# Optimization experiments

Hardware: AMD Instinct MI355X
Metric: run time of the kernel (lower is better)

## Reference

```python
import jax, jax.numpy as jnp
import numpy as np

N, E, DIN, H, C, ED = 50000, 500000, 264, 4, 32, 16
HID = H * C   # 128
OUT = 128
NEG_SLOPE = 0.2
LN_EPS = 1e-5


def _ln(x, g, b):
    mu = jnp.mean(x, axis=-1, keepdims=True)
    var = jnp.mean((x - mu) ** 2, axis=-1, keepdims=True)
    return (x - mu) * jax.lax.rsqrt(var + LN_EPS) * g + b


def _segment_softmax(scores, seg, num_segments):
    # scores: (E, H), seg: (E,) destination node ids
    m = jax.ops.segment_max(scores, seg, num_segments=num_segments)
    m = jnp.where(jnp.isfinite(m), m, 0.0)
    ex = jnp.exp(scores - m[seg])
    s = jax.ops.segment_sum(ex, seg, num_segments=num_segments)
    return ex / (s[seg] + 1e-16)


def _gatv2(x, src, dst, edge_attr, Wl, bl, Wr, br, We, att, bias):
    # GATv2Conv (PyG semantics): lin_l -> source, lin_r -> target, lin_edge (no bias)
    n = x.shape[0]
    xl = (x @ Wl + bl).reshape(n, H, C)          # source transform
    xr = (x @ Wr + br).reshape(n, H, C)          # target transform
    ee = (edge_attr @ We).reshape(-1, H, C)      # (E, H, C)
    m = xl[src] + xr[dst] + ee                   # per-edge pre-activation
    g = jnp.where(m > 0, m, NEG_SLOPE * m)       # leaky_relu(0.2)
    score = jnp.einsum('ehc,hc->eh', g, att)     # (E, H)
    alpha = _segment_softmax(score, dst, n)      # softmax over in-edges of each dst
    msg = xl[src] * alpha[..., None]             # (E, H, C)
    out = jax.ops.segment_sum(msg, dst, num_segments=n)
    return out.reshape(n, HID) + bias


def setup_inputs() -> dict:
    key = jax.random.key(0)
    ks = jax.random.split(key, 16)
    r = lambda k, s: jax.random.normal(k, s, dtype=jnp.float32) * 0.05
    return {
        'x': jax.random.normal(ks[0], (N, DIN), jnp.float32),
        'edge_attr': jax.random.normal(ks[1], (E, ED), jnp.float32),
        'Wl1': r(ks[2], (DIN, HID)), 'bl1': jnp.zeros((HID,), jnp.float32),
        'Wr1': r(ks[3], (DIN, HID)), 'br1': jnp.zeros((HID,), jnp.float32),
        'We1': r(ks[4], (ED, HID)), 'att1': r(ks[5], (H, C)), 'bias1': jnp.zeros((HID,), jnp.float32),
        'Wl2': r(ks[6], (HID, HID)), 'bl2': jnp.zeros((HID,), jnp.float32),
        'Wr2': r(ks[7], (HID, HID)), 'br2': jnp.zeros((HID,), jnp.float32),
        'We2': r(ks[8], (ED, HID)), 'att2': r(ks[9], (H, C)), 'bias2': jnp.zeros((HID,), jnp.float32),
        'Wres': r(ks[10], (DIN, HID)), 'bres': jnp.zeros((HID,), jnp.float32),
        'Wout': r(ks[11], (HID, OUT)), 'bout': jnp.zeros((OUT,), jnp.float32),
        'g1': jnp.ones((HID,), jnp.float32), 'bn1': jnp.zeros((HID,), jnp.float32),
        'g2': jnp.ones((HID,), jnp.float32), 'bn2': jnp.zeros((HID,), jnp.float32),
        'go': jnp.ones((OUT,), jnp.float32), 'bo': jnp.zeros((OUT,), jnp.float32),
        'edge_index': jax.random.randint(ks[12], (2, E), 0, N, dtype=jnp.int32),
    }


def reference(x, edge_attr, Wl1, bl1, Wr1, br1, We1, att1, bias1,
              Wl2, bl2, Wr2, br2, We2, att2, bias2,
              Wres, bres, Wout, bout, g1, bn1, g2, bn2, go, bo, edge_index):
    src, dst = edge_index[0], edge_index[1]
    residual = x @ Wres + bres
    h = _gatv2(x, src, dst, edge_attr, Wl1, bl1, Wr1, br1, We1, att1, bias1)
    h = jax.nn.elu(h)
    h = _ln(h + residual, g1, bn1)
    residual = h
    h = _gatv2(h, src, dst, edge_attr, Wl2, bl2, Wr2, br2, We2, att2, bias2)
    h = jax.nn.elu(h)
    h = _ln(h + residual, g2, bn2)
    context = _ln(h @ Wout + bout, go, bo)
    return context
```

## Files before the change

kernel.cpp:

```cpp
#include <hip/hip_runtime.h>
#include <hip/hip_bf16.h>
#include <math.h>
#include <stdint.h>

#define NN 50000
#define NE 500000
#define DIN 264
#define KP1 288
#define HID 128
#define EDIM 16
#define GS_LD 136

typedef __attribute__((ext_vector_type(8))) short short8;
typedef __attribute__((ext_vector_type(4))) float f32x4;

__device__ __forceinline__ short f2bf(float v) {
    union { float f; unsigned u; } x; x.f = v;
    unsigned r = x.u + 0x7fff + ((x.u >> 16) & 1);
    return (short)(r >> 16);
}
__device__ __forceinline__ float bf2f(short v) {
    union { float f; unsigned u; } x;
    x.u = ((unsigned)(unsigned short)v) << 16;
    return x.f;
}
__device__ __forceinline__ float bflo(unsigned u) {
    union { float f; unsigned u; } x; x.u = u << 16; return x.f;
}
__device__ __forceinline__ float bfhi(unsigned u) {
    union { float f; unsigned u; } x; x.u = u & 0xffff0000u; return x.f;
}
__device__ __forceinline__ unsigned pk2bf(float a, float b) {
    return (unsigned)(unsigned short)f2bf(a) | ((unsigned)(unsigned short)f2bf(b) << 16);
}

__device__ __forceinline__ void gload_lds16(const void* g, void* l) {
    __builtin_amdgcn_global_load_lds(
        (const __attribute__((address_space(1))) unsigned int*)g,
        (__attribute__((address_space(3))) unsigned int*)l, 16, 0, 0);
}

__global__ void k_count(const int* __restrict__ dst, int* __restrict__ cnt) {
    int e = blockIdx.x * blockDim.x + threadIdx.x;
    if (e < NE) atomicAdd(&cnt[dst[e]], 1);
}

__global__ __launch_bounds__(256) void k_scan1(const int* __restrict__ cnt,
                                               int* __restrict__ off, int* __restrict__ bsum) {
    __shared__ int buf[256];
    int b = blockIdx.x, t = threadIdx.x;
    int i = b * 256 + t;
    int v = (i < NN) ? cnt[i] : 0;
    buf[t] = v; __syncthreads();
    for (int s = 1; s < 256; s <<= 1) {
        int u = (t >= s) ? buf[t - s] : 0; __syncthreads();
        buf[t] += u; __syncthreads();
    }
    if (i < NN) off[i + 1] = buf[t];
    if (t == 255) bsum[b] = buf[255];
}

__global__ void k_scan2(int* __restrict__ bsum, int nb) {
    __shared__ int buf[256];
    int t = threadIdx.x;
    int o = (t < nb) ? bsum[t] : 0;
    buf[t] = o; __syncthreads();
    for (int s = 1; s < 256; s <<= 1) {
        int u = (t >= s) ? buf[t - s] : 0; __syncthreads();
        buf[t] += u; __syncthreads();
    }
    if (t < nb) bsum[t] = buf[t] - o;
}

__global__ void k_scan3c(int* __restrict__ off, const int* __restrict__ bsum,
                         int* __restrict__ cur) {
    int j = blockIdx.x * 256 + threadIdx.x;
    if (j > NN) return;
    int v = (j == 0) ? 0 : off[j] + bsum[(j - 1) >> 8];
    off[j] = v;
    if (j < NN) cur[j] = v;
}

__global__ void k_scatter(const int* __restrict__ src, const int* __restrict__ dst,
                          int* __restrict__ cur, int* __restrict__ srcp,
                          int* __restrict__ dstp, int* __restrict__ ey) {
    int e = blockIdx.x * blockDim.x + threadIdx.x;
    if (e < NE) {
        int d = dst[e];
        int p = atomicAdd(&cur[d], 1);
        srcp[p] = src[e];
        dstp[p] = d;
        ey[p] = e;
    }
}

__global__ void k_cvt_x(const float* __restrict__ x, short* __restrict__ xb) {
    int idx = blockIdx.x * 256 + threadIdx.x;
    if (idx >= NN * KP1) return;
    int i = idx / KP1, k = idx - i * KP1;
    xb[idx] = (k < DIN) ? f2bf(x[(size_t)i * DIN + k]) : (short)0;
}

__global__ void k_prep_w(const float* __restrict__ Wl1, const float* __restrict__ Wr1,
                         const float* __restrict__ Wres, const float* __restrict__ Wl2,
                         const float* __restrict__ Wr2, const float* __restrict__ Wout,
                         const float* __restrict__ bl1, const float* __restrict__ br1,
                         const float* __restrict__ bres, const float* __restrict__ bl2,
                         const float* __restrict__ br2,
                         const float* __restrict__ We1, const float* __restrict__ We2,
                         const float* __restrict__ att1, const float* __restrict__ att2,
                         short* __restrict__ Wt1, short* __restrict__ Wt2,
                         short* __restrict__ Wt3, float* __restrict__ bcat1,
                         float* __restrict__ bcat2,
                         short* __restrict__ WeT1, short* __restrict__ WeT2,
                         short* __restrict__ attB1, short* __restrict__ attB2) {
    int idx = blockIdx.x * 256 + threadIdx.x;
    if (idx < 384 * KP1) {
        int n = idx / KP1, k = idx - n * KP1;
        float v = 0.f;
        if (k < DIN) {
            const float* W = (n < 128) ? Wl1 : ((n < 256) ? Wr1 : Wres);
            v = W[(size_t)k * 128 + (n & 127)];
        }
        Wt1[idx] = f2bf(v);
        return;
    }
    idx -= 384 * KP1;
    if (idx < 256 * 128) {
        int n = idx >> 7, k = idx & 127;
        const float* W = (n < 128) ? Wl2 : Wr2;
        Wt2[idx] = f2bf(W[(size_t)k * 128 + (n & 127)]);
        return;
    }
    idx -= 256 * 128;
    if (idx < 128 * 128) {
        int n = idx >> 7, k = idx & 127;
        Wt3[idx] = f2bf(Wout[(size_t)k * 128 + n]);
        return;
    }
    idx -= 128 * 128;
    if (idx < 384) {
        bcat1[idx] = (idx < 128) ? bl1[idx] : ((idx < 256) ? br1[idx - 128] : bres[idx - 256]);
        return;
    }
    idx -= 384;
    if (idx < 256) {
        bcat2[idx] = (idx < 128) ? bl2[idx] : br2[idx - 128];
        return;
    }
    idx -= 256;
    if (idx < 128 * 32) {
        int n = idx >> 5, k = idx & 31;
        WeT1[idx] = (k < EDIM) ? f2bf(We1[(size_t)k * 128 + n]) : (short)0;
        return;
    }
    idx -= 128 * 32;
    if (idx < 128 * 32) {
        int n = idx >> 5, k = idx & 31;
        WeT2[idx] = (k < EDIM) ? f2bf(We2[(size_t)k * 128 + n]) : (short)0;
        return;
    }
    idx -= 128 * 32;
    if (idx < 16 * 128) {
        int n = idx >> 7, k = idx & 127;
        attB1[idx] = (n == (k >> 5)) ? f2bf(att1[k]) : (short)0;
        return;
    }
    idx -= 16 * 128;
    if (idx < 16 * 128) {
        int n = idx >> 7, k = idx & 127;
        attB2[idx] = (n == (k >> 5)) ? f2bf(att2[k]) : (short)0;
    }
}

__global__ __launch_bounds__(256) void k_gather_ea(const int* __restrict__ ey,
                                                   const float* __restrict__ ea,
                                                   short* __restrict__ eaperm) {
    int pos = blockIdx.x * 256 + threadIdx.x;
    if (pos >= NE) return;
    int e = ey[pos];
    const float4* r = (const float4*)(ea + (size_t)e * EDIM);
    float4 v0 = r[0], v1 = r[1], v2 = r[2], v3 = r[3];
    uint4 w0 = make_uint4(pk2bf(v0.x, v0.y), pk2bf(v0.z, v0.w),
                          pk2bf(v1.x, v1.y), pk2bf(v1.z, v1.w));
    uint4 w1 = make_uint4(pk2bf(v2.x, v2.y), pk2bf(v2.z, v2.w),
                          pk2bf(v3.x, v3.y), pk2bf(v3.z, v3.w));
    uint4* o = (uint4*)(eaperm + (size_t)pos * 32);
    o[0] = w0; o[1] = w1;
    o[2] = make_uint4(0, 0, 0, 0);
    o[3] = make_uint4(0, 0, 0, 0);
}

template <bool BF16OUT>
__global__ __launch_bounds__(256) void k_mfma_gemm(const short* __restrict__ A,
                                                   const short* __restrict__ Bt,
                                                   const float* __restrict__ bias,
                                                   float* __restrict__ Cf,
                                                   short* __restrict__ Cb,
                                                   int M, int Kpad, int NS) {
    __shared__ short As[128 * 32];
    __shared__ short Bs[128 * 32];
    int t = threadIdx.x;
    int lane = t & 63, wid = t >> 6;
    int wm = (wid & 1) * 64, wn = (wid >> 1) * 64;
    int cl = lane & 15, quad = lane >> 4;
    int row0 = blockIdx.x * 128;
    int col0 = blockIdx.y * 128;

    f32x4 acc[4][4];
#pragma unroll
    for (int i = 0; i < 4; ++i)
#pragma unroll
        for (int j = 0; j < 4; ++j) acc[i][j] = (f32x4)0.f;

    for (int k0 = 0; k0 < Kpad; k0 += 32) {
#pragma unroll
        for (int r = 0; r < 2; ++r) {
            int c = t + r * 256;
            int m = c >> 2;
            int row = row0 + m; if (row >= M) row = M - 1;
            const char* ga = (const char*)A + ((size_t)row * Kpad + k0) * 2 + (c & 3) * 16;
            gload_lds16(ga, (char*)As + c * 16);
            int n = col0 + m;
            const char* gb = (const char*)Bt + ((size_t)n * Kpad + k0) * 2 + (c & 3) * 16;
            gload_lds16(gb, (char*)Bs + c * 16);
        }
        __syncthreads();

        short8 a[4], b[4];
#pragma unroll
        for (int mi = 0; mi < 4; ++mi)
            a[mi] = *(const short8*)&As[(wm + mi * 16 + cl) * 32 + quad * 8];
#pragma unroll
        for (int ni = 0; ni < 4; ++ni)
            b[ni] = *(const short8*)&Bs[(wn + ni * 16 + cl) * 32 + quad * 8];
#pragma unroll
        for (int mi = 0; mi < 4; ++mi)
#pragma unroll
            for (int ni = 0; ni < 4; ++ni)
                acc[mi][ni] = __builtin_amdgcn_mfma_f32_16x16x32_bf16(a[mi], b[ni], acc[mi][ni], 0, 0, 0);
        __syncthreads();
    }

#pragma unroll
    for (int mi = 0; mi < 4; ++mi)
#pragma unroll
        for (int ni = 0; ni < 4; ++ni) {
            int col = col0 + wn + ni * 16 + cl;
            float bv = bias[col];
#pragma unroll
            for (int r = 0; r < 4; ++r) {
                int row = row0 + wm + mi * 16 + quad * 4 + r;
                if (row < M) {
                    float v = acc[mi][ni][r] + bv;
                    if (BF16OUT) Cb[(size_t)row * NS + col] = f2bf(v);
                    else         Cf[(size_t)row * NS + col] = v;
                }
            }
        }
}

__global__ __launch_bounds__(256) void k_gemm_ln(const short* __restrict__ A,
                                                 const short* __restrict__ Bt,
                                                 const float* __restrict__ bias,
                                                 const float* __restrict__ gamma,
                                                 const float* __restrict__ beta,
                                                 float* __restrict__ out, int M) {
    __shared__ short As[128 * 32];
    __shared__ short Bs[128 * 32];
    __shared__ float redS[128][2];
    int t = threadIdx.x;
    int lane = t & 63, wid = t >> 6;
    int wm = (wid & 1) * 64, wn = (wid >> 1) * 64;
    int cl = lane & 15, quad = lane >> 4;
    int row0 = blockIdx.x * 128;
    int wh = wid >> 1;

    f32x4 acc[4][4];
#pragma unroll
    for (int i = 0; i < 4; ++i)
#pragma unroll
        for (int j = 0; j < 4; ++j) acc[i][j] = (f32x4)0.f;

    for (int k0 = 0; k0 < 128; k0 += 32) {
#pragma unroll
        for (int r = 0; r < 2; ++r) {
            int c = t + r * 256;
            int m = c >> 2;
            int row = row0 + m; if (row >= M) row = M - 1;
            const char* ga = (const char*)A + ((size_t)row * 128 + k0) * 2 + (c & 3) * 16;
            gload_lds16(ga, (char*)As + c * 16);
            const char* gb = (const char*)Bt + ((size_t)m * 128 + k0) * 2 + (c & 3) * 16;
            gload_lds16(gb, (char*)Bs + c * 16);
        }
        __syncthreads();

        short8 a[4], b[4];
#pragma unroll
        for (int mi = 0; mi < 4; ++mi)
            a[mi] = *(const short8*)&As[(wm + mi * 16 + cl) * 32 + quad * 8];
#pragma unroll
        for (int ni = 0; ni < 4; ++ni)
            b[ni] = *(const short8*)&Bs[(wn + ni * 16 + cl) * 32 + quad * 8];
#pragma unroll
        for (int mi = 0; mi < 4; ++mi)
#pragma unroll
            for (int ni = 0; ni < 4; ++ni)
                acc[mi][ni] = __builtin_amdgcn_mfma_f32_16x16x32_bf16(a[mi], b[ni], acc[mi][ni], 0, 0, 0);
        __syncthreads();
    }

    float bv[4], gv[4], bev[4];
#pragma unroll
    for (int ni = 0; ni < 4; ++ni) {
        int col = wn + ni * 16 + cl;
        bv[ni] = bias[col]; gv[ni] = gamma[col]; bev[ni] = beta[col];
    }

    float s[4][4];
#pragma unroll
    for (int mi = 0; mi < 4; ++mi)
#pragma unroll
        for (int r = 0; r < 4; ++r) {
            float v = (acc[mi][0][r] + bv[0]) + (acc[mi][1][r] + bv[1]) +
                      (acc[mi][2][r] + bv[2]) + (acc[mi][3][r] + bv[3]);
            v += __shfl_xor(v, 1, 64);
            v += __shfl_xor(v, 2, 64);
            v += __shfl_xor(v, 4, 64);
            v += __shfl_xor(v, 8, 64);
            s[mi][r] = v;
        }
    if (cl == 0) {
#pragma unroll
        for (int mi = 0; mi < 4; ++mi)
#pragma unroll
            for (int r = 0; r < 4; ++r)
                redS[wm + mi * 16 + quad * 4 + r][wh] = s[mi][r];
    }
    __syncthreads();
    float mean[4][4];
#pragma unroll
    for (int mi = 0; mi < 4; ++mi)
#pragma unroll
        for (int r = 0; r < 4; ++r) {
            int rl = wm + mi * 16 + quad * 4 + r;
            mean[mi][r] = (redS[rl][0] + redS[rl][1]) * (1.f / 128.f);
        }
    __syncthreads();

#pragma unroll
    for (int mi = 0; mi < 4; ++mi)
#pragma unroll
        for (int r = 0; r < 4; ++r) {
            float q = 0.f;
#pragma unroll
            for (int ni = 0; ni < 4; ++ni) {
                float d = acc[mi][ni][r] + bv[ni] - mean[mi][r];
                q = fmaf(d, d, q);
            }
            q += __shfl_xor(q, 1, 64);
            q += __shfl_xor(q, 2, 64);
            q += __shfl_xor(q, 4, 64);
            q += __shfl_xor(q, 8, 64);
            s[mi][r] = q;
        }
    if (cl == 0) {
#pragma unroll
        for (int mi = 0; mi < 4; ++mi)
#pragma unroll
            for (int r = 0; r < 4; ++r)
                redS[wm + mi * 16 + quad * 4 + r][wh] = s[mi][r];
    }
    __syncthreads();

#pragma unroll
    for (int mi = 0; mi < 4; ++mi)
#pragma unroll
        for (int r = 0; r < 4; ++r) {
            int rl = wm + mi * 16 + quad * 4 + r;
            int row = row0 + rl;
            if (row < M) {
                float rstd = rsqrtf((redS[rl][0] + redS[rl][1]) * (1.f / 128.f) + 1e-5f);
#pragma unroll
                for (int ni = 0; ni < 4; ++ni) {
                    int col = wn + ni * 16 + cl;
                    float d = acc[mi][ni][r] + bv[ni] - mean[mi][r];
                    out[(size_t)row * 128 + col] = fmaf(d * rstd, gv[ni], bev[ni]);
                }
            }
        }
}

template <int STRIDE>
__global__ __launch_bounds__(256) void k_edge_score(const short* __restrict__ eaperm,
                                                    const short* __restrict__ WeT,
                                                    const short* __restrict__ attB,
                                                    const int* __restrict__ srcp,
                                                    const int* __restrict__ dstp,
                                                    const short* __restrict__ C,
                                                    float* __restrict__ pe) {
    __shared__ short As[128 * 32];
    __shared__ short Bs[128 * 32];
    __shared__ short Gs[128 * GS_LD];
    __shared__ short Ab[16 * 128];
    __shared__ int sS[128], sD[128];
    int t = threadIdx.x;
    int lane = t & 63, wid = t >> 6;
    int wm = (wid & 1) * 64, wn = (wid >> 1) * 64;
    int cl = lane & 15, quad = lane >> 4;
    long e0 = (long)blockIdx.x * 128;

    if (t < 128) {
        long ep = e0 + t; if (ep >= NE) ep = NE - 1;
        sS[t] = srcp[ep];
        sD[t] = dstp[ep];
    }
    ((uint4*)Ab)[t] = ((const uint4*)attB)[t];

#pragma unroll
    for (int r = 0; r < 2; ++r) {
        int c = t + r * 256;
        int m = c >> 2;
        long row = e0 + m; if (row >= NE) row = NE - 1;
        const char* ga = (const char*)eaperm + row * 64 + (c & 3) * 16;
        gload_lds16(ga, (char*)As + c * 16);
        const char* gb = (const char*)WeT + (size_t)m * 64 + (c & 3) * 16;
        gload_lds16(gb, (char*)Bs + c * 16);
    }
    __syncthreads();

    f32x4 acc[4][4];
#pragma unroll
    for (int i = 0; i < 4; ++i)
#pragma unroll
        for (int j = 0; j < 4; ++j) acc[i][j] = (f32x4)0.f;
    {
        short8 a[4], b[4];
#pragma unroll
        for (int mi = 0; mi < 4; ++mi)
            a[mi] = *(const short8*)&As[(wm + mi * 16 + cl) * 32 + quad * 8];
#pragma unroll
        for (int ni = 0; ni < 4; ++ni)
            b[ni] = *(const short8*)&Bs[(wn + ni * 16 + cl) * 32 + quad * 8];
#pragma unroll
        for (int mi = 0; mi < 4; ++mi)
#pragma unroll
            for (int ni = 0; ni < 4; ++ni)
                acc[mi][ni] = __builtin_amdgcn_mfma_f32_16x16x32_bf16(a[mi], b[ni], acc[mi][ni], 0, 0, 0);
    }

#pragma unroll
    for (int mi = 0; mi < 4; ++mi) {
#pragma unroll
        for (int r = 0; r < 4; ++r) {
            int eloc = wm + mi * 16 + quad * 4 + r;
            const short* xlr = C + (size_t)sS[eloc] * STRIDE;
            const short* xrr = C + (size_t)sD[eloc] * STRIDE + 128;
#pragma unroll
            for (int ni = 0; ni < 4; ++ni) {
                int f = wn + ni * 16 + cl;
                float g = acc[mi][ni][r] + bf2f(xlr[f]) + bf2f(xrr[f]);
                g = fmaxf(g, 0.2f * g);
                Gs[eloc * GS_LD + f] = f2bf(g);
            }
        }
    }
    __syncthreads();

    f32x4 sacc[2];
    sacc[0] = (f32x4)0.f; sacc[1] = (f32x4)0.f;
    int em0 = wid * 32;
#pragma unroll
    for (int mt = 0; mt < 2; ++mt) {
#pragma unroll
        for (int ks = 0; ks < 4; ++ks) {
            short8 ag = *(const short8*)&Gs[(em0 + mt * 16 + cl) * GS_LD + ks * 32 + quad * 8];
            short8 bg = *(const short8*)&Ab[cl * 128 + ks * 32 + quad * 8];
            sacc[mt] = __builtin_amdgcn_mfma_f32_16x16x32_bf16(ag, bg, sacc[mt], 0, 0, 0);
        }
    }

    if (cl < 4) {
#pragma unroll
        for (int mt = 0; mt < 2; ++mt) {
#pragma unroll
            for (int r = 0; r < 4; ++r) {
                long epos = e0 + em0 + mt * 16 + quad * 4 + r;
                if (epos < NE) pe[epos * 4 + cl] = __expf(sacc[mt][r]);
            }
        }
    }
}

template <int STRIDE>
__global__ __launch_bounds__(256) void k_fused_agg(const int* __restrict__ off,
                                                   const int* __restrict__ srcp,
                                                   const float* __restrict__ pe,
                                                   const short* __restrict__ C,
                                                   const short* __restrict__ resid, int rstride,
                                                   const float* __restrict__ bias,
                                                   const float* __restrict__ gamma,
                                                   const float* __restrict__ beta,
                                                   short* __restrict__ outb) {
    int t = threadIdx.x;
    int w = t >> 6, l = t & 63;
    int f0 = (l >> 4) * 32 + (l & 15) * 2;
    int fp = f0 >> 1;
    int hd = l >> 4;

    float2 bs2 = ((const float2*)bias)[fp];
    float2 gv = ((const float2*)gamma)[fp];
    float2 bev = ((const float2*)beta)[fp];

    int n0 = (blockIdx.x * 4 + w) * 4;
    int nend = n0 + 4; if (nend > NN) nend = NN;

    for (int i = n0; i < nend; ++i) {
        unsigned rp = *(const unsigned*)&resid[(size_t)i * rstride + f0];
        int b0 = off[i], b1 = off[i + 1];

        float lA = 0.f, aA0 = 0.f, aA1 = 0.f;
        float lB = 0.f, aB0 = 0.f, aB1 = 0.f;
        int pos = b0;
        int sA = 0, sB = 0; float pA = 0.f, pB = 0.f;
        bool have = (pos + 2 <= b1);
        if (have) {
            sA = srcp[pos]; sB = srcp[pos + 1];
            pA = pe[(size_t)pos * 4 + hd]; pB = pe[(size_t)(pos + 1) * 4 + hd];
        }
        while (have) {
            bool haven = (pos + 4 <= b1);
            int nsA = 0, nsB = 0; float npA = 0.f, npB = 0.f;
            if (haven) {
                nsA = srcp[pos + 2]; nsB = srcp[pos + 3];
                npA = pe[(size_t)(pos + 2) * 4 + hd]; npB = pe[(size_t)(pos + 3) * 4 + hd];
            }
            unsigned xlA = *(const unsigned*)&C[(size_t)sA * STRIDE + f0];
            unsigned xlB = *(const unsigned*)&C[(size_t)sB * STRIDE + f0];
            lA += pA; lB += pB;
            aA0 = fmaf(pA, bflo(xlA), aA0);
            aA1 = fmaf(pA, bfhi(xlA), aA1);
            aB0 = fmaf(pB, bflo(xlB), aB0);
            aB1 = fmaf(pB, bfhi(xlB), aB1);
            pos += 2;
            sA = nsA; sB = nsB; pA = npA; pB = npB;
            have = haven;
        }
        if (pos < b1) {
            int s1 = srcp[pos];
            float p1 = pe[(size_t)pos * 4 + hd];
            unsigned xlv = *(const unsigned*)&C[(size_t)s1 * STRIDE + f0];
            lA += p1;
            aA0 = fmaf(p1, bflo(xlv), aA0);
            aA1 = fmaf(p1, bfhi(xlv), aA1);
        }
        float l_run = lA + lB;
        float acc0 = aA0 + aB0, acc1 = aA1 + aB1;

        float inv = 1.f / (l_run + 1e-16f);
        float o0 = fmaf(acc0, inv, bs2.x);
        float o1 = fmaf(acc1, inv, bs2.y);
        o0 = o0 > 0.f ? o0 : (__expf(o0) - 1.f);
        o1 = o1 > 0.f ? o1 : (__expf(o1) - 1.f);
        float v0 = o0 + bflo(rp), v1 = o1 + bfhi(rp);
        float s = v0 + v1;
#pragma unroll
        for (int o = 32; o > 0; o >>= 1) s += __shfl_xor(s, o, 64);
        float mean = s * (1.f / 128.f);
        float d0 = v0 - mean, d1 = v1 - mean;
        float q = fmaf(d0, d0, d1 * d1);
#pragma unroll
        for (int o = 32; o > 0; o >>= 1) q += __shfl_xor(q, o, 64);
        float rstd = rsqrtf(q * (1.f / 128.f) + 1e-5f);
        float r0 = fmaf(d0 * rstd, gv.x, bev.x);
        float r1 = fmaf(d1 * rstd, gv.y, bev.y);
        unsigned op = (unsigned)(unsigned short)f2bf(r0) |
                      (((unsigned)(unsigned short)f2bf(r1)) << 16);
        *(unsigned*)&outb[(size_t)i * 128 + f0] = op;
    }
}

extern "C" void kernel_launch(void* const* d_in, const int* in_sizes, int n_in,
                              void* d_out, int out_size, void* d_ws, size_t ws_size,
                              hipStream_t stream) {
    (void)in_sizes; (void)n_in; (void)out_size; (void)ws_size;
    const float* x     = (const float*)d_in[0];
    const float* ea    = (const float*)d_in[1];
    const float* Wl1   = (const float*)d_in[2];
    const float* bl1   = (const float*)d_in[3];
    const float* Wr1   = (const float*)d_in[4];
    const float* br1   = (const float*)d_in[5];
    const float* We1   = (const float*)d_in[6];
    const float* att1  = (const float*)d_in[7];
    const float* bias1 = (const float*)d_in[8];
    const float* Wl2   = (const float*)d_in[9];
    const float* bl2   = (const float*)d_in[10];
    const float* Wr2   = (const float*)d_in[11];
    const float* br2   = (const float*)d_in[12];
    const float* We2   = (const float*)d_in[13];
    const float* att2  = (const float*)d_in[14];
    const float* bias2 = (const float*)d_in[15];
    const float* Wres  = (const float*)d_in[16];
    const float* bres  = (const float*)d_in[17];
    const float* Wout  = (const float*)d_in[18];
    const float* bout  = (const float*)d_in[19];
    const float* g1    = (const float*)d_in[20];
    const float* bn1   = (const float*)d_in[21];
    const float* g2    = (const float*)d_in[22];
    const float* bn2   = (const float*)d_in[23];
    const float* go    = (const float*)d_in[24];
    const float* bo    = (const float*)d_in[25];
    const int*   ei    = (const int*)d_in[26];
    const int* srcv = ei;
    const int* dstv = ei + NE;
    float* outp = (float*)d_out;

    char* p = (char*)d_ws;
    auto carve = [&](size_t bytes) {
        char* r = p;
        p += (bytes + 255) & ~(size_t)255;
        return r;
    };
    short* xb    = (short*)carve((size_t)NN * KP1 * 2);
    short* Wt1   = (short*)carve((size_t)384 * KP1 * 2);
    short* Wt2   = (short*)carve((size_t)256 * 128 * 2);
    short* Wt3   = (short*)carve((size_t)128 * 128 * 2);
    short* WeT1  = (short*)carve((size_t)128 * 32 * 2);
    short* WeT2  = (short*)carve((size_t)128 * 32 * 2);
    short* attB1 = (short*)carve((size_t)16 * 128 * 2);
    short* attB2 = (short*)carve((size_t)16 * 128 * 2);
    float* bcat1 = (float*)carve(384 * 4);
    float* bcat2 = (float*)carve(256 * 4);
    short* C1    = (short*)carve((size_t)NN * 384 * 2);
    short* h1b   = (short*)carve((size_t)NN * 128 * 2);
    short* h2b   = (short*)carve((size_t)NN * 128 * 2);
    int* off     = (int*)carve((size_t)(NN + 1) * 4);
    int* cur     = (int*)carve((size_t)NN * 4);
    int* bsum    = (int*)carve(256 * 4);
    int* srcp    = (int*)carve((size_t)NE * 4);
    int* dstp    = (int*)carve((size_t)NE * 4);
    int* ey      = (int*)carve((size_t)NE * 4);
    short* eaperm = (short*)carve((size_t)NE * 32 * 2);
    float* pe    = (float*)carve((size_t)NE * 4 * 4);

    short* C2 = C1;

    const int NB = (NN + 255) / 256;

    hipMemsetAsync(cur, 0, (size_t)NN * 4, stream);
    k_count<<<(NE + 255) / 256, 256, 0, stream>>>(dstv, cur);
    k_scan1<<<NB, 256, 0, stream>>>(cur, off, bsum);
    k_scan2<<<1, 256, 0, stream>>>(bsum, NB);
    k_scan3c<<<(NN + 256) / 256, 256, 0, stream>>>(off, bsum, cur);
    k_scatter<<<(NE + 255) / 256, 256, 0, stream>>>(srcv, dstv, cur, srcp, dstp, ey);

    k_cvt_x<<<((size_t)NN * KP1 + 255) / 256, 256, 0, stream>>>(x, xb);
    int prep_total = 384 * KP1 + 256 * 128 + 128 * 128 + 384 + 256 + 2 * 128 * 32 + 2 * 16 * 128;
    k_prep_w<<<(prep_total + 255) / 256, 256, 0, stream>>>(Wl1, Wr1, Wres, Wl2, Wr2, Wout,
                                                           bl1, br1, bres, bl2, br2,
                                                           We1, We2, att1, att2,
                                                           Wt1, Wt2, Wt3, bcat1, bcat2,
                                                           WeT1, WeT2, attB1, attB2);
    k_gather_ea<<<(NE + 255) / 256, 256, 0, stream>>>(ey, ea, eaperm);

    int mb  = (NN + 127) / 128;
    int ebk = (NE + 127) / 128;
    int gagg = (NN + 15) / 16;

    k_mfma_gemm<true><<<dim3(mb, 3), 256, 0, stream>>>(xb, Wt1, bcat1, nullptr, C1, NN, KP1, 384);
    k_edge_score<384><<<ebk, 256, 0, stream>>>(eaperm, WeT1, attB1, srcp, dstp, C1, pe);
    k_fused_agg<384><<<gagg, 256, 0, stream>>>(off, srcp, pe, C1,
                                               C1 + 256, 384, bias1, g1, bn1, h1b);
    k_mfma_gemm<true><<<dim3(mb, 2), 256, 0, stream>>>(h1b, Wt2, bcat2, nullptr, C2, NN, 128, 256);
    k_edge_score<256><<<ebk, 256, 0, stream>>>(eaperm, WeT2, attB2, srcp, dstp, C2, pe);
    k_fused_agg<256><<<gagg, 256, 0, stream>>>(off, srcp, pe, C2,
                                               h1b, 128, bias2, g2, bn2, h2b);
    k_gemm_ln<<<mb, 256, 0, stream>>>(h2b, Wt3, bout, go, bo, outp, NN);
}
```

Before: 508.7 us.

## Compute edge scores in registers via transposed MFMA, drop LDS staging

The edge-score kernel now computes the transposed product (features × edges) so each lane holds contiguous features of one edge. It loads operands directly from global memory instead of staging them in LDS. The attention dot product is done with FMAs and cross-quad shuffles rather than a second MFMA over an LDS buffer of bf16 activations, which removes both __syncthreads and the intermediate bf16 rounding. Gathered xl/xr rows are read as 4-wide vectors. The risk is more uncoalesced global loads per lane and more shuffle work.

```diff
diff --git a/kernel.cpp b/kernel.cpp
--- a/kernel.cpp
+++ b/kernel.cpp
@@ -9,7 +9,6 @@
 #define KP1 288
 #define HID 128
 #define EDIM 16
-#define GS_LD 136
 
 typedef __attribute__((ext_vector_type(8))) short short8;
 typedef __attribute__((ext_vector_type(4))) float f32x4;
@@ -108,12 +107,10 @@
                          const float* __restrict__ bres, const float* __restrict__ bl2,
                          const float* __restrict__ br2,
                          const float* __restrict__ We1, const float* __restrict__ We2,
-                         const float* __restrict__ att1, const float* __restrict__ att2,
                          short* __restrict__ Wt1, short* __restrict__ Wt2,
                          short* __restrict__ Wt3, float* __restrict__ bcat1,
                          float* __restrict__ bcat2,
-                         short* __restrict__ WeT1, short* __restrict__ WeT2,
-                         short* __restrict__ attB1, short* __restrict__ attB2) {
+                         short* __restrict__ WeT1, short* __restrict__ WeT2) {
     int idx = blockIdx.x * 256 + threadIdx.x;
     if (idx < 384 * KP1) {
         int n = idx / KP1, k = idx - n * KP1;
@@ -158,18 +155,6 @@
     if (idx < 128 * 32) {
         int n = idx >> 5, k = idx & 31;
         WeT2[idx] = (k < EDIM) ? f2bf(We2[(size_t)k * 128 + n]) : (short)0;
-        return;
-    }
-    idx -= 128 * 32;
-    if (idx < 16 * 128) {
-        int n = idx >> 7, k = idx & 127;
-        attB1[idx] = (n == (k >> 5)) ? f2bf(att1[k]) : (short)0;
-        return;
-    }
-    idx -= 16 * 128;
-    if (idx < 16 * 128) {
-        int n = idx >> 7, k = idx & 127;
-        attB2[idx] = (n == (k >> 5)) ? f2bf(att2[k]) : (short)0;
     }
 }
 
@@ -394,100 +379,81 @@
 template <int STRIDE>
 __global__ __launch_bounds__(256) void k_edge_score(const short* __restrict__ eaperm,
                                                     const short* __restrict__ WeT,
-                                                    const short* __restrict__ attB,
+                                                    const float* __restrict__ att,
                                                     const int* __restrict__ srcp,
                                                     const int* __restrict__ dstp,
                                                     const short* __restrict__ C,
                                                     float* __restrict__ pe) {
-    __shared__ short As[128 * 32];
-    __shared__ short Bs[128 * 32];
-    __shared__ short Gs[128 * GS_LD];
-    __shared__ short Ab[16 * 128];
-    __shared__ int sS[128], sD[128];
     int t = threadIdx.x;
     int lane = t & 63, wid = t >> 6;
     int wm = (wid & 1) * 64, wn = (wid >> 1) * 64;
     int cl = lane & 15, quad = lane >> 4;
     long e0 = (long)blockIdx.x * 128;
 
-    if (t < 128) {
-        long ep = e0 + t; if (ep >= NE) ep = NE - 1;
-        sS[t] = srcp[ep];
-        sD[t] = dstp[ep];
-    }
-    ((uint4*)Ab)[t] = ((const uint4*)attB)[t];
-
-#pragma unroll
-    for (int r = 0; r < 2; ++r) {
-        int c = t + r * 256;
-        int m = c >> 2;
-        long row = e0 + m; if (row >= NE) row = NE - 1;
-        const char* ga = (const char*)eaperm + row * 64 + (c & 3) * 16;
-        gload_lds16(ga, (char*)As + c * 16);
-        const char* gb = (const char*)WeT + (size_t)m * 64 + (c & 3) * 16;
-        gload_lds16(gb, (char*)Bs + c * 16);
-    }
-    __syncthreads();
+    short8 a[4];
+#pragma unroll
+    for (int mi = 0; mi < 4; ++mi)
+        a[mi] = *(const short8*)&WeT[(size_t)(wm + mi * 16 + cl) * 32 + quad * 8];
+
+    short8 b[4];
+    int esrc[4], edst[4];
+#pragma unroll
+    for (int ni = 0; ni < 4; ++ni) {
+        long e = e0 + wn + ni * 16 + cl; if (e >= NE) e = NE - 1;
+        b[ni] = *(const short8*)&eaperm[e * 32 + quad * 8];
+        esrc[ni] = srcp[e];
+        edst[ni] = dstp[e];
+    }
+
+    float attv[4][4];
+#pragma unroll
+    for (int mi = 0; mi < 4; ++mi)
+#pragma unroll
+        for (int r = 0; r < 4; ++r)
+            attv[mi][r] = att[wm + mi * 16 + quad * 4 + r];
 
     f32x4 acc[4][4];
 #pragma unroll
     for (int i = 0; i < 4; ++i)
 #pragma unroll
         for (int j = 0; j < 4; ++j) acc[i][j] = (f32x4)0.f;
-    {
-        short8 a[4], b[4];
-#pragma unroll
-        for (int mi = 0; mi < 4; ++mi)
-            a[mi] = *(const short8*)&As[(wm + mi * 16 + cl) * 32 + quad * 8];
+#pragma unroll
+    for (int mi = 0; mi < 4; ++mi)
 #pragma unroll
         for (int ni = 0; ni < 4; ++ni)
-            b[ni] = *(const short8*)&Bs[(wn + ni * 16 + cl) * 32 + quad * 8];
-#pragma unroll
-        for (int mi = 0; mi < 4; ++mi)
-#pragma unroll
-            for (int ni = 0; ni < 4; ++ni)
-                acc[mi][ni] = __builtin_amdgcn_mfma_f32_16x16x32_bf16(a[mi], b[ni], acc[mi][ni], 0, 0, 0);
-    }
-
-#pragma unroll
-    for (int mi = 0; mi < 4; ++mi) {
-#pragma unroll
-        for (int r = 0; r < 4; ++r) {
-            int eloc = wm + mi * 16 + quad * 4 + r;
-            const short* xlr = C + (size_t)sS[eloc] * STRIDE;
-            const short* xrr = C + (size_t)sD[eloc] * STRIDE + 128;
-#pragma unroll
-            for (int ni = 0; ni < 4; ++ni) {
-                int f = wn + ni * 16 + cl;
-                float g = acc[mi][ni][r] + bf2f(xlr[f]) + bf2f(xrr[f]);
+            acc[mi][ni] = __builtin_amdgcn_mfma_f32_16x16x32_bf16(a[mi], b[ni], acc[mi][ni], 0, 0, 0);
+
+    int hbase = wm >> 5;
+#pragma unroll
+    for (int ni = 0; ni < 4; ++ni) {
+        const short* xlr = C + (size_t)esrc[ni] * STRIDE;
+        const short* xrr = C + (size_t)edst[ni] * STRIDE + 128;
+        uint2 xl2[4], xr2[4];
+#pragma unroll
+        for (int mi = 0; mi < 4; ++mi) {
+            int f0 = wm + mi * 16 + quad * 4;
+            xl2[mi] = *(const uint2*)&xlr[f0];
+            xr2[mi] = *(const uint2*)&xrr[f0];
+        }
+        float p0 = 0.f, p1 = 0.f;
+#pragma unroll
+        for (int mi = 0; mi < 4; ++mi) {
+            float xlv[4] = { bflo(xl2[mi].x), bfhi(xl2[mi].x), bflo(xl2[mi].y), bfhi(xl2[mi].y) };
+            float xrv[4] = { bflo(xr2[mi].x), bfhi(xr2[mi].x), bflo(xr2[mi].y), bfhi(xr2[mi].y) };
+#pragma unroll
+            for (int r = 0; r < 4; ++r) {
+                float g = acc[mi][ni][r] + xlv[r] + xrv[r];
                 g = fmaxf(g, 0.2f * g);
-                Gs[eloc * GS_LD + f] = f2bf(g);
+                if (mi < 2) p0 = fmaf(attv[mi][r], g, p0);
+                else        p1 = fmaf(attv[mi][r], g, p1);
             }
         }
-    }
-    __syncthreads();
-
-    f32x4 sacc[2];
-    sacc[0] = (f32x4)0.f; sacc[1] = (f32x4)0.f;
-    int em0 = wid * 32;
-#pragma unroll
-    for (int mt = 0; mt < 2; ++mt) {
-#pragma unroll
-        for (int ks = 0; ks < 4; ++ks) {
-            short8 ag = *(const short8*)&Gs[(em0 + mt * 16 + cl) * GS_LD + ks * 32 + quad * 8];
-            short8 bg = *(const short8*)&Ab[cl * 128 + ks * 32 + quad * 8];
-            sacc[mt] = __builtin_amdgcn_mfma_f32_16x16x32_bf16(ag, bg, sacc[mt], 0, 0, 0);
-        }
-    }
-
-    if (cl < 4) {
-#pragma unroll
-        for (int mt = 0; mt < 2; ++mt) {
-#pragma unroll
-            for (int r = 0; r < 4; ++r) {
-                long epos = e0 + em0 + mt * 16 + quad * 4 + r;
-                if (epos < NE) pe[epos * 4 + cl] = __expf(sacc[mt][r]);
-            }
+        p0 += __shfl_xor(p0, 16, 64); p0 += __shfl_xor(p0, 32, 64);
+        p1 += __shfl_xor(p1, 16, 64); p1 += __shfl_xor(p1, 32, 64);
+        long e = e0 + wn + ni * 16 + cl;
+        if (e < NE) {
+            if (quad == 0)      pe[e * 4 + hbase]     = __expf(p0);
+            else if (quad == 1) pe[e * 4 + hbase + 1] = __expf(p1);
         }
     }
 }
@@ -627,8 +593,6 @@
     short* Wt3   = (short*)carve((size_t)128 * 128 * 2);
     short* WeT1  = (short*)carve((size_t)128 * 32 * 2);
     short* WeT2  = (short*)carve((size_t)128 * 32 * 2);
-    short* attB1 = (short*)carve((size_t)16 * 128 * 2);
-    short* attB2 = (short*)carve((size_t)16 * 128 * 2);
     float* bcat1 = (float*)carve(384 * 4);
     float* bcat2 = (float*)carve(256 * 4);
     short* C1    = (short*)carve((size_t)NN * 384 * 2);
@@ -655,12 +619,12 @@
     k_scatter<<<(NE + 255) / 256, 256, 0, stream>>>(srcv, dstv, cur, srcp, dstp, ey);
 
     k_cvt_x<<<((size_t)NN * KP1 + 255) / 256, 256, 0, stream>>>(x, xb);
-    int prep_total = 384 * KP1 + 256 * 128 + 128 * 128 + 384 + 256 + 2 * 128 * 32 + 2 * 16 * 128;
+    int prep_total = 384 * KP1 + 256 * 128 + 128 * 128 + 384 + 256 + 2 * 128 * 32;
     k_prep_w<<<(prep_total + 255) / 256, 256, 0, stream>>>(Wl1, Wr1, Wres, Wl2, Wr2, Wout,
                                                            bl1, br1, bres, bl2, br2,
-                                                           We1, We2, att1, att2,
+                                                           We1, We2,
                                                            Wt1, Wt2, Wt3, bcat1, bcat2,
-                                                           WeT1, WeT2, attB1, attB2);
+                                                           WeT1, WeT2);
     k_gather_ea<<<(NE + 255) / 256, 256, 0, stream>>>(ey, ea, eaperm);
 
     int mb  = (NN + 127) / 128;
@@ -668,11 +632,11 @@
     int gagg = (NN + 15) / 16;
 
     k_mfma_gemm<true><<<dim3(mb, 3), 256, 0, stream>>>(xb, Wt1, bcat1, nullptr, C1, NN, KP1, 384);
-    k_edge_score<384><<<ebk, 256, 0, stream>>>(eaperm, WeT1, attB1, srcp, dstp, C1, pe);
+    k_edge_score<384><<<ebk, 256, 0, stream>>>(eaperm, WeT1, att1, srcp, dstp, C1, pe);
     k_fused_agg<384><<<gagg, 256, 0, stream>>>(off, srcp, pe, C1,
                                                C1 + 256, 384, bias1, g1, bn1, h1b);
     k_mfma_gemm<true><<<dim3(mb, 2), 256, 0, stream>>>(h1b, Wt2, bcat2, nullptr, C2, NN, 128, 256);
-    k_edge_score<256><<<ebk, 256, 0, stream>>>(eaperm, WeT2, attB2, srcp, dstp, C2, pe);
+    k_edge_score<256><<<ebk, 256, 0, stream>>>(eaperm, WeT2, att2, srcp, dstp, C2, pe);
     k_fused_agg<256><<<gagg, 256, 0, stream>>>(off, srcp, pe, C2,
                                                h1b, 128, bias2, g2, bn2, h2b);
     k_gemm_ln<<<mb, 256, 0, stream>>>(h2b, Wt3, bout, go, bo, outp, NN);
```

Measured after the change: 522.6 us. +2.7%, slower.

## Widen edge-score blocks to 512 threads and load MFMA operands straight to registers

Applied to the files above, without the earlier changes.

The edge-score kernel now runs 8 waves per 128-edge block instead of 4. Each wave computes a 64x32 output tile instead of 64x64, and one 16-edge tile of the attention projection instead of two. The edge-attribute and edge-weight operands are loaded from global memory directly into registers instead of staging through LDS, which removes a shared buffer and one barrier phase. The attention operand is padded to stride 136. The aim is more latency hiding for the per-edge gathers of source and destination rows, at the cost of more threads per block and unstaged global loads.

```diff
diff --git a/kernel.cpp b/kernel.cpp
--- a/kernel.cpp
+++ b/kernel.cpp
@@ -9,7 +9,6 @@
 #define KP1 288
 #define HID 128
 #define EDIM 16
-#define GS_LD 136
 
 typedef __attribute__((ext_vector_type(8))) short short8;
 typedef __attribute__((ext_vector_type(4))) float f32x4;
@@ -392,21 +391,20 @@
 }
 
 template <int STRIDE>
-__global__ __launch_bounds__(256) void k_edge_score(const short* __restrict__ eaperm,
+__global__ __launch_bounds__(512) void k_edge_score(const short* __restrict__ eaperm,
                                                     const short* __restrict__ WeT,
                                                     const short* __restrict__ attB,
                                                     const int* __restrict__ srcp,
                                                     const int* __restrict__ dstp,
                                                     const short* __restrict__ C,
                                                     float* __restrict__ pe) {
-    __shared__ short As[128 * 32];
-    __shared__ short Bs[128 * 32];
-    __shared__ short Gs[128 * GS_LD];
-    __shared__ short Ab[16 * 128];
+    __shared__ short Gs[128 * 136];
+    __shared__ short Ab[16 * 136];
     __shared__ int sS[128], sD[128];
     int t = threadIdx.x;
     int lane = t & 63, wid = t >> 6;
-    int wm = (wid & 1) * 64, wn = (wid >> 1) * 64;
+    int wm2 = (wid & 1) * 64;
+    int wn2 = (wid >> 1) * 32;
     int cl = lane & 15, quad = lane >> 4;
     long e0 = (long)blockIdx.x * 128;
 
@@ -414,80 +412,66 @@
         long ep = e0 + t; if (ep >= NE) ep = NE - 1;
         sS[t] = srcp[ep];
         sD[t] = dstp[ep];
-    }
-    ((uint4*)Ab)[t] = ((const uint4*)attB)[t];
-
-#pragma unroll
-    for (int r = 0; r < 2; ++r) {
-        int c = t + r * 256;
-        int m = c >> 2;
-        long row = e0 + m; if (row >= NE) row = NE - 1;
-        const char* ga = (const char*)eaperm + row * 64 + (c & 3) * 16;
-        gload_lds16(ga, (char*)As + c * 16);
-        const char* gb = (const char*)WeT + (size_t)m * 64 + (c & 3) * 16;
-        gload_lds16(gb, (char*)Bs + c * 16);
-    }
+    } else if (t < 384) {
+        int u = t - 128;
+        int rr = u >> 4, cc = (u & 15) * 8;
+        *(short8*)&Ab[rr * 136 + cc] = *(const short8*)&attB[rr * 128 + cc];
+    }
+
+    short8 a[4], b[2];
+#pragma unroll
+    for (int mi = 0; mi < 4; ++mi) {
+        long e = e0 + wm2 + mi * 16 + cl; if (e >= NE) e = NE - 1;
+        a[mi] = *(const short8*)&eaperm[e * 32 + quad * 8];
+    }
+#pragma unroll
+    for (int ni = 0; ni < 2; ++ni)
+        b[ni] = *(const short8*)&WeT[(size_t)(wn2 + ni * 16 + cl) * 32 + quad * 8];
+
+    f32x4 acc[4][2];
+#pragma unroll
+    for (int i = 0; i < 4; ++i) { acc[i][0] = (f32x4)0.f; acc[i][1] = (f32x4)0.f; }
+#pragma unroll
+    for (int mi = 0; mi < 4; ++mi)
+#pragma unroll
+        for (int ni = 0; ni < 2; ++ni)
+            acc[mi][ni] = __builtin_amdgcn_mfma_f32_16x16x32_bf16(a[mi], b[ni], acc[mi][ni], 0, 0, 0);
     __syncthreads();
 
-    f32x4 acc[4][4];
-#pragma unroll
-    for (int i = 0; i < 4; ++i)
-#pragma unroll
-        for (int j = 0; j < 4; ++j) acc[i][j] = (f32x4)0.f;
-    {
-        short8 a[4], b[4];
-#pragma unroll
-        for (int mi = 0; mi < 4; ++mi)
-            a[mi] = *(const short8*)&As[(wm + mi * 16 + cl) * 32 + quad * 8];
-#pragma unroll
-        for (int ni = 0; ni < 4; ++ni)
-            b[ni] = *(const short8*)&Bs[(wn + ni * 16 + cl) * 32 + quad * 8];
-#pragma unroll
-        for (int mi = 0; mi < 4; ++mi)
-#pragma unroll
-            for (int ni = 0; ni < 4; ++ni)
-                acc[mi][ni] = __builtin_amdgcn_mfma_f32_16x16x32_bf16(a[mi], b[ni], acc[mi][ni], 0, 0, 0);
-    }
-
 #pragma unroll
     for (int mi = 0; mi < 4; ++mi) {
 #pragma unroll
         for (int r = 0; r < 4; ++r) {
-            int eloc = wm + mi * 16 + quad * 4 + r;
+            int eloc = wm2 + mi * 16 + quad * 4 + r;
             const short* xlr = C + (size_t)sS[eloc] * STRIDE;
             const short* xrr = C + (size_t)sD[eloc] * STRIDE + 128;
-#pragma unroll
-            for (int ni = 0; ni < 4; ++ni) {
-                int f = wn + ni * 16 + cl;
-                float g = acc[mi][ni][r] + bf2f(xlr[f]) + bf2f(xrr[f]);
-                g = fmaxf(g, 0.2f * g);
-                Gs[eloc * GS_LD + f] = f2bf(g);
-            }
+            int f0 = wn2 + cl, f1 = wn2 + 16 + cl;
+            float xl0 = bf2f(xlr[f0]), xr0 = bf2f(xrr[f0]);
+            float xl1 = bf2f(xlr[f1]), xr1 = bf2f(xrr[f1]);
+            float g0 = acc[mi][0][r] + xl0 + xr0;
+            float g1 = acc[mi][1][r] + xl1 + xr1;
+            g0 = fmaxf(g0, 0.2f * g0);
+            g1 = fmaxf(g1, 0.2f * g1);
+            Gs[eloc * 136 + f0] = f2bf(g0);
+            Gs[eloc * 136 + f1] = f2bf(g1);
         }
     }
     __syncthreads();
 
-    f32x4 sacc[2];
-    sacc[0] = (f32x4)0.f; sacc[1] = (f32x4)0.f;
-    int em0 = wid * 32;
-#pragma unroll
-    for (int mt = 0; mt < 2; ++mt) {
-#pragma unroll
-        for (int ks = 0; ks < 4; ++ks) {
-            short8 ag = *(const short8*)&Gs[(em0 + mt * 16 + cl) * GS_LD + ks * 32 + quad * 8];
-            short8 bg = *(const short8*)&Ab[cl * 128 + ks * 32 + quad * 8];
-            sacc[mt] = __builtin_amdgcn_mfma_f32_16x16x32_bf16(ag, bg, sacc[mt], 0, 0, 0);
-        }
+    f32x4 sacc = (f32x4)0.f;
+    int em0 = wid * 16;
+#pragma unroll
+    for (int ks = 0; ks < 4; ++ks) {
+        short8 ag = *(const short8*)&Gs[(em0 + cl) * 136 + ks * 32 + quad * 8];
+        short8 bg = *(const short8*)&Ab[cl * 136 + ks * 32 + quad * 8];
+        sacc = __builtin_amdgcn_mfma_f32_16x16x32_bf16(ag, bg, sacc, 0, 0, 0);
     }
 
     if (cl < 4) {
 #pragma unroll
-        for (int mt = 0; mt < 2; ++mt) {
-#pragma unroll
-            for (int r = 0; r < 4; ++r) {
-                long epos = e0 + em0 + mt * 16 + quad * 4 + r;
-                if (epos < NE) pe[epos * 4 + cl] = __expf(sacc[mt][r]);
-            }
+        for (int r = 0; r < 4; ++r) {
+            long epos = e0 + em0 + quad * 4 + r;
+            if (epos < NE) pe[epos * 4 + cl] = __expf(sacc[r]);
         }
     }
 }
@@ -668,11 +652,11 @@
     int gagg = (NN + 15) / 16;
 
     k_mfma_gemm<true><<<dim3(mb, 3), 256, 0, stream>>>(xb, Wt1, bcat1, nullptr, C1, NN, KP1, 384);
-    k_edge_score<384><<<ebk, 256, 0, stream>>>(eaperm, WeT1, attB1, srcp, dstp, C1, pe);
+    k_edge_score<384><<<ebk, 512, 0, stream>>>(eaperm, WeT1, attB1, srcp, dstp, C1, pe);
     k_fused_agg<384><<<gagg, 256, 0, stream>>>(off, srcp, pe, C1,
                                                C1 + 256, 384, bias1, g1, bn1, h1b);
     k_mfma_gemm<true><<<dim3(mb, 2), 256, 0, stream>>>(h1b, Wt2, bcat2, nullptr, C2, NN, 128, 256);
-    k_edge_score<256><<<ebk, 256, 0, stream>>>(eaperm, WeT2, attB2, srcp, dstp, C2, pe);
+    k_edge_score<256><<<ebk, 512, 0, stream>>>(eaperm, WeT2, attB2, srcp, dstp, C2, pe);
     k_fused_agg<256><<<gagg, 256, 0, stream>>>(off, srcp, pe, C2,
                                                h1b, 128, bias2, g2, bn2, h2b);
     k_gemm_ln<<<mb, 256, 0, stream>>>(h2b, Wt3, bout, go, bo, outp, NN);
```

After: 483.8 us. -4.9%, faster.
